# Performance work log

Measured on AMD Instinct MI355X. Metric: run time of the kernel, lower is better.

The kernel has to match this reference:

```python
import jax, jax.numpy as jnp
import numpy as np


def _linear(x, W, b):
    # torch nn.Linear: y = x @ W.T + b, W is [out, in]
    return x @ W.T + b


def _sage_layer(x, edge_index, Ws, bs, Wn, bn):
    # GraphSAGE: mean-aggregate neighbor features via scatter-add, then two linears.
    src, tgt = edge_index[0], edge_index[1]
    N = x.shape[0]
    agg = jax.ops.segment_sum(x[src], tgt, num_segments=N)            # [N, D]
    deg = jax.ops.segment_sum(jnp.ones(src.shape, x.dtype), tgt, num_segments=N)  # [N]
    neighbor_mean = agg / jnp.maximum(deg, 1.0)[:, None]
    return _linear(x, Ws, bs) + _linear(neighbor_mean, Wn, bn)


def setup_inputs() -> dict:
    key = jax.random.key(0)
    ks = jax.random.split(key, 16)
    N, ATTR, H, OUT, E = 50000, 125, 128, 128, 800000
    IN = ATTR + 3
    s = 0.05
    inp = {
        "attr_features": jax.random.normal(ks[0], (N, ATTR), jnp.float32),
        "clustering_coefficient": jax.random.uniform(ks[1], (N, 1), jnp.float32),
        "bidirectional_links_ratio": jax.random.uniform(ks[2], (N, 1), jnp.float32),
        "exist_nodes": jnp.ones((N,), jnp.float32),
        "W_in": s * jax.random.normal(ks[3], (H, IN), jnp.float32),
        "b_in": s * jax.random.normal(ks[4], (H,), jnp.float32),
        "W1_self": s * jax.random.normal(ks[5], (H, H), jnp.float32),
        "b1_self": s * jax.random.normal(ks[6], (H,), jnp.float32),
        "W1_neigh": s * jax.random.normal(ks[7], (H, H), jnp.float32),
        "b1_neigh": s * jax.random.normal(ks[8], (H,), jnp.float32),
        "W2_self": s * jax.random.normal(ks[9], (OUT, H), jnp.float32),
        "b2_self": s * jax.random.normal(ks[10], (OUT,), jnp.float32),
        "W2_neigh": s * jax.random.normal(ks[11], (OUT, H), jnp.float32),
        "b2_neigh": s * jax.random.normal(ks[12], (OUT,), jnp.float32),
        "edge_index": jax.random.randint(ks[13], (2, E), 0, N, jnp.int64),
    }
    return inp


def reference(attr_features, clustering_coefficient, bidirectional_links_ratio,
              exist_nodes, W_in, b_in, W1_self, b1_self, W1_neigh, b1_neigh,
              W2_self, b2_self, W2_neigh, b2_neigh, edge_index):
    exist_col = exist_nodes[:, None]                                   # [N, 1]
    x = jnp.concatenate(
        [attr_features, clustering_coefficient, bidirectional_links_ratio, exist_col],
        axis=1)                                                        # [N, attr_dim+3]
    x = jax.nn.relu(_linear(x, W_in, b_in))                            # dropout=0 -> identity
    x = _sage_layer(x, edge_index, W1_self, b1_self, W1_neigh, b1_neigh)
    x = jax.nn.relu(x)
    x = x * exist_col
    x = _sage_layer(x, edge_index, W2_self, b2_self, W2_neigh, b2_neigh)
    return x * exist_col
```

## Files before the change

kernel.cpp:

```cpp
#include <hip/hip_runtime.h>

typedef __attribute__((ext_vector_type(8))) short short8;
typedef __attribute__((ext_vector_type(4))) float floatx4;

__device__ inline unsigned short f2bf(float f) {
    unsigned u = __float_as_uint(f);
    u += 0x7fffu + ((u >> 16) & 1u);
    return (unsigned short)(u >> 16);
}

__device__ inline short8 pack8(const float4 a, const float4 b) {
    short8 r;
    r[0] = (short)f2bf(a.x); r[1] = (short)f2bf(a.y);
    r[2] = (short)f2bf(a.z); r[3] = (short)f2bf(a.w);
    r[4] = (short)f2bf(b.x); r[5] = (short)f2bf(b.y);
    r[6] = (short)f2bf(b.z); r[7] = (short)f2bf(b.w);
    return r;
}

#define CHUNK_CAP 6144
#define BTILE 4096


__global__ __launch_bounds__(256, 3) void gemm0_bin(
    const float* __restrict__ attr, const float* __restrict__ cc,
    const float* __restrict__ bl, const float* __restrict__ ex,
    const float* __restrict__ Wf, const float* __restrict__ bias,
    unsigned short* __restrict__ out_bf,
    const int* __restrict__ e, int* __restrict__ cursor,
    unsigned* __restrict__ packed_out,
    int N, int ATTR, int E, int nbin) {
    __shared__ __align__(16) char smem[2 * BTILE * 4 + 4 * 256 * 4];
    int t = threadIdx.x;

    if ((int)blockIdx.x < nbin) {
        unsigned* buf  = (unsigned*)smem;
        unsigned* sbuf = buf + BTILE;
        int* hist  = (int*)(sbuf + BTILE);
        int* offs  = hist + 256;
        int* gbase = offs + 256;
        int* lcur  = gbase + 256;
        int e0 = blockIdx.x * BTILE;
        int cnt = min(BTILE, E - e0);
        hist[t] = 0;
        __syncthreads();
        for (int j = t; j < cnt; j += 256) {
            unsigned src = (unsigned)e[e0 + j];
            unsigned tgt = (unsigned)e[E + e0 + j];
            buf[j] = (src << 16) | tgt;
            atomicAdd(&hist[tgt >> 8], 1);
        }
        __syncthreads();
        offs[t] = hist[t];
        __syncthreads();
        for (int o = 1; o < 256; o <<= 1) {
            int v = (t >= o) ? offs[t - o] : 0;
            __syncthreads();
            offs[t] += v;
            __syncthreads();
        }
        int excl = offs[t] - hist[t];
        offs[t] = excl;
        lcur[t] = excl;
        gbase[t] = (hist[t] > 0) ? t * CHUNK_CAP + atomicAdd(&cursor[t], hist[t]) : 0;
        __syncthreads();
        for (int j = t; j < cnt; j += 256) {
            unsigned v = buf[j];
            int c = (v >> 8) & 0xFF;
            int p = atomicAdd(&lcur[c], 1);
            sbuf[p] = v;
        }
        __syncthreads();
        int wv = t >> 6, lane = t & 63;
        for (int c = wv; c < 256; c += 4) {
            int n = hist[c], lo = offs[c], gb = gbase[c];
            for (int j = lane; j < n; j += 64)
                packed_out[gb + j] = sbuf[lo + j];
        }
        return;
    }

    unsigned short* lx = (unsigned short*)smem;
    int lane = t & 63;
    int w = t >> 6;
    int node0 = ((int)blockIdx.x - nbin) * 64;
    int n_off = w * 32;
    int q = lane >> 4;
    int m16 = lane & 15;

    short8 bf[2][4];
    #pragma unroll
    for (int nt = 0; nt < 2; ++nt)
        #pragma unroll
        for (int kk = 0; kk < 4; ++kk) {
            const float* p = Wf + (n_off + nt * 16 + m16) * 128 + kk * 32 + q * 8;
            bf[nt][kk] = pack8(*(const float4*)p, *(const float4*)(p + 4));
        }

    floatx4 acc[4][2];
    #pragma unroll
    for (int nt = 0; nt < 2; ++nt) {
        float bv = bias[n_off + nt * 16 + m16];
        floatx4 b4 = {bv, bv, bv, bv};
        #pragma unroll
        for (int mt = 0; mt < 4; ++mt) acc[mt][nt] = b4;
    }

    for (int i = 0; i < 32; ++i) {
        int idx = t + 256 * i;
        int nd = idx >> 7, col = idx & 127;
        int row = node0 + nd;
        float v = 0.0f;
        if (row < N) {
            if (col < ATTR)           v = attr[(size_t)row * ATTR + col];
            else if (col == ATTR)     v = cc[row];
            else if (col == ATTR + 1) v = bl[row];
            else                      v = ex[row];
        }
        lx[nd * 136 + col] = f2bf(v);
    }
    __syncthreads();

    #pragma unroll
    for (int kk = 0; kk < 4; ++kk) {
        short8 a[4];
        #pragma unroll
        for (int mt = 0; mt < 4; ++mt)
            a[mt] = *(const short8*)(lx + (mt * 16 + m16) * 136 + kk * 32 + q * 8);
        #pragma unroll
        for (int mt = 0; mt < 4; ++mt) {
            acc[mt][0] = __builtin_amdgcn_mfma_f32_16x16x32_bf16(a[mt], bf[0][kk], acc[mt][0], 0, 0, 0);
            acc[mt][1] = __builtin_amdgcn_mfma_f32_16x16x32_bf16(a[mt], bf[1][kk], acc[mt][1], 0, 0, 0);
        }
    }

    for (int mt = 0; mt < 4; ++mt) {
        int rbase = node0 + mt * 16 + q * 4;
        for (int r = 0; r < 4; ++r) {
            int rr = rbase + r;
            if (rr >= N) continue;
            for (int nt = 0; nt < 2; ++nt) {
                float v = fmaxf(acc[mt][nt][r], 0.0f);
                out_bf[(size_t)rr * 128 + n_off + nt * 16 + m16] = f2bf(v);
            }
        }
    }
}


__global__ __launch_bounds__(256) void chunk_csr(const unsigned* __restrict__ packed,
                                                 const int* __restrict__ cursor,
                                                 uint2* __restrict__ rows2,
                                                 int* __restrict__ colv, int N) {
    __shared__ int hist[256], offs[256], lcnt[256];
    __shared__ int sbuf[CHUNK_CAP];
    int c = blockIdx.x;
    int base = c * CHUNK_CAP;
    int cnt = cursor[c];
    int t = threadIdx.x;
    hist[t] = 0;
    __syncthreads();
    for (int j = t; j < cnt; j += 256)
        atomicAdd(&hist[packed[base + j] & 255u], 1);
    __syncthreads();
    offs[t] = hist[t];
    __syncthreads();
    for (int o = 1; o < 256; o <<= 1) {
        int v = (t >= o) ? offs[t - o] : 0;
        __syncthreads();
        offs[t] += v;
        __syncthreads();
    }
    int excl = offs[t] - hist[t];
    offs[t] = excl;
    lcnt[t] = 0;
    __syncthreads();
    int node = c * 256 + t;
    if (node < N) {
        uint2 r;
        r.x = base + excl;
        r.y = base + excl + hist[t];
        rows2[node] = r;
    }
    for (int j = t; j < cnt; j += 256) {
        unsigned v = packed[base + j];
        int nd = v & 255u;
        int p = offs[nd] + atomicAdd(&lcnt[nd], 1);
        sbuf[p] = v >> 16;
    }
    __syncthreads();
    for (int j = t; j < cnt; j += 256) colv[base + j] = sbuf[j];
}


__global__ __launch_bounds__(256) void agg_mean(const unsigned short* __restrict__ x,
                                                const uint2* __restrict__ rows2,
                                                const int* __restrict__ colv,
                                                unsigned short* __restrict__ nm, int N) {
    int wid = (blockIdx.x * 256 + threadIdx.x) >> 6;
    int lane = threadIdx.x & 63;
    if (wid >= N) return;
    uint2 r = rows2[wid];
    int s0 = r.x, s1 = r.y;
    int deg = s1 - s0;
    int mn = deg < 64 ? deg : 64;
    int cvec = (lane < mn) ? colv[s0 + lane] : 0;
    int quarter = lane >> 4;
    int cl = (lane & 15) * 8;
    float a0 = 0.f, a1 = 0.f, a2 = 0.f, a3 = 0.f;
    float a4 = 0.f, a5 = 0.f, a6 = 0.f, a7 = 0.f;
    int lim = mn - 1;
    for (int j = 0; j < mn; j += 32) {
        uint4 v[8];
        #pragma unroll
        for (int u = 0; u < 8; ++u) {
            int ei = j + 4 * u + quarter;
            int idx = (ei <= lim) ? ei : lim;
            int s = __shfl(cvec, idx, 64);
            v[u] = *(const uint4*)(x + (size_t)s * 128 + cl);
        }
        #pragma unroll
        for (int u = 0; u < 8; ++u) {
            int ei = j + 4 * u + quarter;
            if (ei <= lim) {
                a0 += __uint_as_float(v[u].x << 16);
                a1 += __uint_as_float(v[u].x & 0xffff0000u);
                a2 += __uint_as_float(v[u].y << 16);
                a3 += __uint_as_float(v[u].y & 0xffff0000u);
                a4 += __uint_as_float(v[u].z << 16);
                a5 += __uint_as_float(v[u].z & 0xffff0000u);
                a6 += __uint_as_float(v[u].w << 16);
                a7 += __uint_as_float(v[u].w & 0xffff0000u);
            }
        }
    }
    for (int e = s0 + 64; e < s1; e += 4) {
        int ei = e + quarter;
        int idx = (ei < s1) ? ei : s1 - 1;
        int s = colv[idx];
        uint4 v = *(const uint4*)(x + (size_t)s * 128 + cl);
        if (ei < s1) {
            a0 += __uint_as_float(v.x << 16);
            a1 += __uint_as_float(v.x & 0xffff0000u);
            a2 += __uint_as_float(v.y << 16);
            a3 += __uint_as_float(v.y & 0xffff0000u);
            a4 += __uint_as_float(v.z << 16);
            a5 += __uint_as_float(v.z & 0xffff0000u);
            a6 += __uint_as_float(v.w << 16);
            a7 += __uint_as_float(v.w & 0xffff0000u);
        }
    }
    a0 += __shfl_xor(a0, 16, 64); a0 += __shfl_xor(a0, 32, 64);
    a1 += __shfl_xor(a1, 16, 64); a1 += __shfl_xor(a1, 32, 64);
    a2 += __shfl_xor(a2, 16, 64); a2 += __shfl_xor(a2, 32, 64);
    a3 += __shfl_xor(a3, 16, 64); a3 += __shfl_xor(a3, 32, 64);
    a4 += __shfl_xor(a4, 16, 64); a4 += __shfl_xor(a4, 32, 64);
    a5 += __shfl_xor(a5, 16, 64); a5 += __shfl_xor(a5, 32, 64);
    a6 += __shfl_xor(a6, 16, 64); a6 += __shfl_xor(a6, 32, 64);
    a7 += __shfl_xor(a7, 16, 64); a7 += __shfl_xor(a7, 32, 64);
    if (quarter == 0) {
        float inv = 1.0f / (float)(deg > 1 ? deg : 1);
        a0 *= inv; a1 *= inv; a2 *= inv; a3 *= inv;
        a4 *= inv; a5 *= inv; a6 *= inv; a7 *= inv;
        uint4 o;
        o.x = ((unsigned)f2bf(a1) << 16) | (unsigned)f2bf(a0);
        o.y = ((unsigned)f2bf(a3) << 16) | (unsigned)f2bf(a2);
        o.z = ((unsigned)f2bf(a5) << 16) | (unsigned)f2bf(a4);
        o.w = ((unsigned)f2bf(a7) << 16) | (unsigned)f2bf(a6);
        *(uint4*)(nm + (size_t)wid * 128 + cl) = o;
    }
}


__global__ __launch_bounds__(256, 3) void gemm_fused(
    const unsigned short* __restrict__ X0, const unsigned short* __restrict__ X1,
    const float* __restrict__ W0f, const float* __restrict__ W1f,
    const float* __restrict__ b0, const float* __restrict__ b1,
    const float* __restrict__ ex,
    unsigned short* __restrict__ obf, float* __restrict__ of32,
    int N, int relu) {
    __shared__ unsigned short lx[64 * 136];
    int tid = threadIdx.x;
    int lane = tid & 63;
    int w = tid >> 6;
    int node0 = blockIdx.x * 64;
    int n_off = w * 32;
    int q = lane >> 4;
    int m16 = lane & 15;

    short8 bf0[2][4], bf1[2][4];
    #pragma unroll
    for (int nt = 0; nt < 2; ++nt)
        #pragma unroll
        for (int kk = 0; kk < 4; ++kk) {
            const float* p0 = W0f + (n_off + nt * 16 + m16) * 128 + kk * 32 + q * 8;
            bf0[nt][kk] = pack8(*(const float4*)p0, *(const float4*)(p0 + 4));
            const float* p1 = W1f + (n_off + nt * 16 + m16) * 128 + kk * 32 + q * 8;
            bf1[nt][kk] = pack8(*(const float4*)p1, *(const float4*)(p1 + 4));
        }

    floatx4 acc[4][2];
    #pragma unroll
    for (int nt = 0; nt < 2; ++nt) {
        int col = n_off + nt * 16 + m16;
        float bv = b0[col] + b1[col];
        floatx4 b4 = {bv, bv, bv, bv};
        #pragma unroll
        for (int mt = 0; mt < 4; ++mt) acc[mt][nt] = b4;
    }

    for (int ph = 0; ph < 2; ++ph) {
        const unsigned short* X = ph ? X1 : X0;
        for (int i = 0; i < 4; ++i) {
            int c = tid + 256 * i;
            int nd = c >> 4, ck = c & 15;
            short8 v = {0, 0, 0, 0, 0, 0, 0, 0};
            if (node0 + nd < N) v = *(const short8*)(X + (size_t)(node0 + nd) * 128 + ck * 8);
            *(short8*)(lx + nd * 136 + ck * 8) = v;
        }
        __syncthreads();
        #pragma unroll
        for (int kk = 0; kk < 4; ++kk) {
            short8 a[4];
            #pragma unroll
            for (int mt = 0; mt < 4; ++mt)
                a[mt] = *(const short8*)(lx + (mt * 16 + m16) * 136 + kk * 32 + q * 8);
            #pragma unroll
            for (int mt = 0; mt < 4; ++mt) {
                const short8* p0 = ph ? &bf1[0][kk] : &bf0[0][kk];
                const short8* p1 = ph ? &bf1[1][kk] : &bf0[1][kk];
                acc[mt][0] = __builtin_amdgcn_mfma_f32_16x16x32_bf16(a[mt], *p0, acc[mt][0], 0, 0, 0);
                acc[mt][1] = __builtin_amdgcn_mfma_f32_16x16x32_bf16(a[mt], *p1, acc[mt][1], 0, 0, 0);
            }
        }
        __syncthreads();
    }

    for (int mt = 0; mt < 4; ++mt) {
        int rbase = node0 + mt * 16 + q * 4;
        for (int r = 0; r < 4; ++r) {
            int rr = rbase + r;
            if (rr >= N) continue;
            float e = ex ? ex[rr] : 1.0f;
            for (int nt = 0; nt < 2; ++nt) {
                float v = acc[mt][nt][r];
                if (relu) v = fmaxf(v, 0.0f);
                v *= e;
                int col = n_off + nt * 16 + m16;
                if (obf) obf[(size_t)rr * 128 + col] = f2bf(v);
                else     of32[(size_t)rr * 128 + col] = v;
            }
        }
    }
}


extern "C" void kernel_launch(void* const* d_in, const int* in_sizes, int n_in,
                              void* d_out, int out_size, void* d_ws, size_t ws_size,
                              hipStream_t stream) {
    const float* attr = (const float*)d_in[0];
    const float* cc   = (const float*)d_in[1];
    const float* bl   = (const float*)d_in[2];
    const float* ex   = (const float*)d_in[3];
    const float* w_in = (const float*)d_in[4];
    const float* b_in = (const float*)d_in[5];
    const float* w1s  = (const float*)d_in[6];
    const float* b1s  = (const float*)d_in[7];
    const float* w1n  = (const float*)d_in[8];
    const float* b1n  = (const float*)d_in[9];
    const float* w2s  = (const float*)d_in[10];
    const float* b2s  = (const float*)d_in[11];
    const float* w2n  = (const float*)d_in[12];
    const float* b2n  = (const float*)d_in[13];
    const int*   eidx = (const int*)d_in[14];

    int N = in_sizes[3];
    int ATTR = in_sizes[0] / N;
    int E = in_sizes[14] / 2;
    int Npad = ((N + 63) / 64) * 64;
    int nchunk = (N + 255) / 256;
    int ntilesE = (E + BTILE - 1) / BTILE;
    int gblk = Npad / 64;

    char* ws = (char*)d_ws;
    size_t off = 0;
    auto alloc = [&](size_t bytes) -> char* {
        off = (off + 255) & ~(size_t)255;
        char* p = ws + off;
        off += bytes;
        return p;
    };
    unsigned short* x1 = (unsigned short*)alloc((size_t)Npad * 128 * 2);
    unsigned short* x2 = (unsigned short*)alloc((size_t)Npad * 128 * 2);
    unsigned short* nm = (unsigned short*)alloc((size_t)Npad * 128 * 2);
    int* colv        = (int*)alloc((size_t)nchunk * CHUNK_CAP * 4);
    unsigned* packed = (unsigned*)alloc((size_t)nchunk * CHUNK_CAP * 4);
    uint2* rows2     = (uint2*)alloc((size_t)N * 8);
    int* cursor      = (int*)alloc(256 * 4);

    hipMemsetAsync(cursor, 0, 256 * sizeof(int), stream);

    gemm0_bin<<<ntilesE + gblk, 256, 0, stream>>>(attr, cc, bl, ex, w_in, b_in, x1,
                                                  eidx, cursor, packed,
                                                  N, ATTR, E, ntilesE);
    chunk_csr<<<nchunk, 256, 0, stream>>>(packed, cursor, rows2, colv, N);
    agg_mean<<<(N + 3) / 4, 256, 0, stream>>>(x1, rows2, colv, nm, N);
    gemm_fused<<<gblk, 256, 0, stream>>>(x1, nm, w1s, w1n, b1s, b1n, ex,
                                         x2, (float*)nullptr, N, 1);
    agg_mean<<<(N + 3) / 4, 256, 0, stream>>>(x2, rows2, colv, nm, N);
    gemm_fused<<<gblk, 256, 0, stream>>>(x2, nm, w2s, w2n, b2s, b2n, ex,
                                         (unsigned short*)nullptr, (float*)d_out, N, 0);
}
```

Before: 264.4 us.

## Widen CSR chunks, persist binning blocks, pre-convert weights, stage attr rows

Edge binning now uses 128 chunks of 512 nodes with a new packed encoding, and a fixed pool of at most 256 blocks loops over the edge tiles. The chunk_csr kernel builds 512-node CSR rows with a two-per-thread scan. Extra blocks in the first kernel convert the layer weights to bf16 once and pre-sum the biases, so the fused GEMMs load short8 directly instead of converting per block. The input GEMM stages attr rows into LDS with coalesced float4 loads instead of strided scalar reads. This raises LDS use per block, which may lower occupancy.

```diff
diff --git a/kernel.cpp b/kernel.cpp
--- a/kernel.cpp
+++ b/kernel.cpp
@@ -9,17 +9,9 @@
     return (unsigned short)(u >> 16);
 }
 
-__device__ inline short8 pack8(const float4 a, const float4 b) {
-    short8 r;
-    r[0] = (short)f2bf(a.x); r[1] = (short)f2bf(a.y);
-    r[2] = (short)f2bf(a.z); r[3] = (short)f2bf(a.w);
-    r[4] = (short)f2bf(b.x); r[5] = (short)f2bf(b.y);
-    r[6] = (short)f2bf(b.z); r[7] = (short)f2bf(b.w);
-    return r;
-}
-
-#define CHUNK_CAP 6144
+#define CHUNK_CAP 12288
 #define BTILE 4096
+#define NPREP 256
 
 
 __global__ __launch_bounds__(256, 3) void gemm0_bin(
@@ -29,72 +21,114 @@
     unsigned short* __restrict__ out_bf,
     const int* __restrict__ e, int* __restrict__ cursor,
     unsigned* __restrict__ packed_out,
-    int N, int ATTR, int E, int nbin) {
-    __shared__ __align__(16) char smem[2 * BTILE * 4 + 4 * 256 * 4];
+    const float* __restrict__ w1s, const float* __restrict__ w1n,
+    const float* __restrict__ w2s, const float* __restrict__ w2n,
+    const float* __restrict__ b1s, const float* __restrict__ b1n,
+    const float* __restrict__ b2s, const float* __restrict__ b2n,
+    unsigned short* __restrict__ wb, float* __restrict__ biasf,
+    int N, int ATTR, int E, int ntilesE, int nbin) {
+    __shared__ __align__(16) char smem[49408];
     int t = threadIdx.x;
-
-    if ((int)blockIdx.x < nbin) {
+    int bid = blockIdx.x;
+
+    if (bid < nbin) {
         unsigned* buf  = (unsigned*)smem;
         unsigned* sbuf = buf + BTILE;
         int* hist  = (int*)(sbuf + BTILE);
-        int* offs  = hist + 256;
-        int* gbase = offs + 256;
-        int* lcur  = gbase + 256;
-        int e0 = blockIdx.x * BTILE;
-        int cnt = min(BTILE, E - e0);
-        hist[t] = 0;
-        __syncthreads();
-        for (int j = t; j < cnt; j += 256) {
-            unsigned src = (unsigned)e[e0 + j];
-            unsigned tgt = (unsigned)e[E + e0 + j];
-            buf[j] = (src << 16) | tgt;
-            atomicAdd(&hist[tgt >> 8], 1);
-        }
-        __syncthreads();
-        offs[t] = hist[t];
-        __syncthreads();
-        for (int o = 1; o < 256; o <<= 1) {
-            int v = (t >= o) ? offs[t - o] : 0;
-            __syncthreads();
-            offs[t] += v;
-            __syncthreads();
-        }
-        int excl = offs[t] - hist[t];
-        offs[t] = excl;
-        lcur[t] = excl;
-        gbase[t] = (hist[t] > 0) ? t * CHUNK_CAP + atomicAdd(&cursor[t], hist[t]) : 0;
-        __syncthreads();
-        for (int j = t; j < cnt; j += 256) {
-            unsigned v = buf[j];
-            int c = (v >> 8) & 0xFF;
-            int p = atomicAdd(&lcur[c], 1);
-            sbuf[p] = v;
-        }
-        __syncthreads();
-        int wv = t >> 6, lane = t & 63;
-        for (int c = wv; c < 256; c += 4) {
-            int n = hist[c], lo = offs[c], gb = gbase[c];
-            for (int j = lane; j < n; j += 64)
-                packed_out[gb + j] = sbuf[lo + j];
+        int* offs  = hist + 128;
+        int* gbase = offs + 128;
+        int* lcur  = gbase + 128;
+        for (int tile = bid; tile < ntilesE; tile += nbin) {
+            int e0 = tile * BTILE;
+            int cnt = min(BTILE, E - e0);
+            if (t < 128) hist[t] = 0;
+            __syncthreads();
+            for (int j = t; j < cnt; j += 256) {
+                unsigned src = (unsigned)e[e0 + j];
+                unsigned tgt = (unsigned)e[E + e0 + j];
+                unsigned c = tgt >> 9;
+                buf[j] = (c << 25) | (src << 9) | (tgt & 511u);
+                atomicAdd(&hist[c], 1);
+            }
+            __syncthreads();
+            if (t < 128) offs[t] = hist[t];
+            __syncthreads();
+            for (int o = 1; o < 128; o <<= 1) {
+                int v = (t < 128 && t >= o) ? offs[t - o] : 0;
+                __syncthreads();
+                if (t < 128) offs[t] += v;
+                __syncthreads();
+            }
+            if (t < 128) {
+                int excl = offs[t] - hist[t];
+                offs[t] = excl;
+                lcur[t] = excl;
+                gbase[t] = (hist[t] > 0) ? t * CHUNK_CAP + atomicAdd(&cursor[t], hist[t]) : 0;
+            }
+            __syncthreads();
+            for (int j = t; j < cnt; j += 256) {
+                unsigned v = buf[j];
+                int c = v >> 25;
+                int p = atomicAdd(&lcur[c], 1);
+                sbuf[p] = v;
+            }
+            __syncthreads();
+            int wv = t >> 6, lane = t & 63;
+            for (int c = wv; c < 128; c += 4) {
+                int n = hist[c], lo = offs[c], gb = gbase[c];
+                for (int j = lane; j < n; j += 64)
+                    packed_out[gb + j] = sbuf[lo + j];
+            }
+            __syncthreads();
         }
         return;
     }
 
-    unsigned short* lx = (unsigned short*)smem;
+    if (bid < nbin + NPREP) {
+        int pb = bid - nbin;
+        int idx = pb * 256 + t;
+        int m = idx >> 14, j = idx & 16383;
+        const float* src = (m == 0) ? w1s : (m == 1) ? w1n : (m == 2) ? w2s : w2n;
+        wb[idx] = f2bf(src[j]);
+        if (pb == 0 && t < 128) {
+            biasf[t]       = b1s[t] + b1n[t];
+            biasf[128 + t] = b2s[t] + b2n[t];
+        }
+        return;
+    }
+
+    float* sflat = (float*)smem;
+    unsigned short* lx = (unsigned short*)(smem + 32000);
     int lane = t & 63;
     int w = t >> 6;
-    int node0 = ((int)blockIdx.x - nbin) * 64;
+    int node0 = (bid - nbin - NPREP) * 64;
     int n_off = w * 32;
     int q = lane >> 4;
     int m16 = lane & 15;
 
+    int nrow = N - node0; nrow = nrow > 64 ? 64 : (nrow < 0 ? 0 : nrow);
+    int nelem = nrow * ATTR;
+    {
+        const float* abase = attr + (size_t)node0 * ATTR;
+        int nv = nelem >> 2;
+        const float4* src4 = (const float4*)abase;
+        for (int i = t; i < nv; i += 256) ((float4*)sflat)[i] = src4[i];
+        for (int i = (nv << 2) + t; i < nelem; i += 256) sflat[i] = abase[i];
+    }
+
     short8 bf[2][4];
     #pragma unroll
     for (int nt = 0; nt < 2; ++nt)
         #pragma unroll
         for (int kk = 0; kk < 4; ++kk) {
             const float* p = Wf + (n_off + nt * 16 + m16) * 128 + kk * 32 + q * 8;
-            bf[nt][kk] = pack8(*(const float4*)p, *(const float4*)(p + 4));
+            float4 aa = *(const float4*)p, bb = *(const float4*)(p + 4);
+            short8 r;
+            r[0] = (short)f2bf(aa.x); r[1] = (short)f2bf(aa.y);
+            r[2] = (short)f2bf(aa.z); r[3] = (short)f2bf(aa.w);
+            r[4] = (short)f2bf(bb.x); r[5] = (short)f2bf(bb.y);
+            r[6] = (short)f2bf(bb.z); r[7] = (short)f2bf(bb.w);
+            bf[nt][kk] = r;
         }
 
     floatx4 acc[4][2];
@@ -105,6 +139,7 @@
         #pragma unroll
         for (int mt = 0; mt < 4; ++mt) acc[mt][nt] = b4;
     }
+    __syncthreads();
 
     for (int i = 0; i < 32; ++i) {
         int idx = t + 256 * i;
@@ -112,7 +147,7 @@
         int row = node0 + nd;
         float v = 0.0f;
         if (row < N) {
-            if (col < ATTR)           v = attr[(size_t)row * ATTR + col];
+            if (col < ATTR)           v = sflat[nd * ATTR + col];
             else if (col == ATTR)     v = cc[row];
             else if (col == ATTR + 1) v = bl[row];
             else                      v = ex[row];
@@ -152,41 +187,47 @@
                                                  const int* __restrict__ cursor,
                                                  uint2* __restrict__ rows2,
                                                  int* __restrict__ colv, int N) {
-    __shared__ int hist[256], offs[256], lcnt[256];
+    __shared__ int hist[512], offs[512], lcnt[512], pp[256];
     __shared__ int sbuf[CHUNK_CAP];
     int c = blockIdx.x;
     int base = c * CHUNK_CAP;
     int cnt = cursor[c];
     int t = threadIdx.x;
     hist[t] = 0;
+    hist[t + 256] = 0;
     __syncthreads();
     for (int j = t; j < cnt; j += 256)
-        atomicAdd(&hist[packed[base + j] & 255u], 1);
-    __syncthreads();
-    offs[t] = hist[t];
+        atomicAdd(&hist[packed[base + j] & 511u], 1);
+    __syncthreads();
+    int a0 = hist[2 * t], a1 = hist[2 * t + 1];
+    pp[t] = a0 + a1;
     __syncthreads();
     for (int o = 1; o < 256; o <<= 1) {
-        int v = (t >= o) ? offs[t - o] : 0;
+        int v = (t >= o) ? pp[t - o] : 0;
         __syncthreads();
-        offs[t] += v;
+        pp[t] += v;
         __syncthreads();
     }
-    int excl = offs[t] - hist[t];
-    offs[t] = excl;
-    lcnt[t] = 0;
-    __syncthreads();
-    int node = c * 256 + t;
-    if (node < N) {
-        uint2 r;
-        r.x = base + excl;
-        r.y = base + excl + hist[t];
-        rows2[node] = r;
+    int excl = pp[t] - (a0 + a1);
+    offs[2 * t] = excl;
+    offs[2 * t + 1] = excl + a0;
+    lcnt[2 * t] = 0;
+    lcnt[2 * t + 1] = 0;
+    __syncthreads();
+    for (int j = t; j < 512; j += 256) {
+        int node = c * 512 + j;
+        if (node < N) {
+            uint2 r;
+            r.x = base + offs[j];
+            r.y = base + offs[j] + hist[j];
+            rows2[node] = r;
+        }
     }
     for (int j = t; j < cnt; j += 256) {
         unsigned v = packed[base + j];
-        int nd = v & 255u;
-        int p = offs[nd] + atomicAdd(&lcnt[nd], 1);
-        sbuf[p] = v >> 16;
+        int node = v & 511u;
+        int p = offs[node] + atomicAdd(&lcnt[node], 1);
+        sbuf[p] = (v >> 9) & 0xFFFFu;
     }
     __syncthreads();
     for (int j = t; j < cnt; j += 256) colv[base + j] = sbuf[j];
@@ -274,9 +315,8 @@
 
 __global__ __launch_bounds__(256, 3) void gemm_fused(
     const unsigned short* __restrict__ X0, const unsigned short* __restrict__ X1,
-    const float* __restrict__ W0f, const float* __restrict__ W1f,
-    const float* __restrict__ b0, const float* __restrict__ b1,
-    const float* __restrict__ ex,
+    const unsigned short* __restrict__ W0, const unsigned short* __restrict__ W1,
+    const float* __restrict__ bias, const float* __restrict__ ex,
     unsigned short* __restrict__ obf, float* __restrict__ of32,
     int N, int relu) {
     __shared__ unsigned short lx[64 * 136];
@@ -293,17 +333,14 @@
     for (int nt = 0; nt < 2; ++nt)
         #pragma unroll
         for (int kk = 0; kk < 4; ++kk) {
-            const float* p0 = W0f + (n_off + nt * 16 + m16) * 128 + kk * 32 + q * 8;
-            bf0[nt][kk] = pack8(*(const float4*)p0, *(const float4*)(p0 + 4));
-            const float* p1 = W1f + (n_off + nt * 16 + m16) * 128 + kk * 32 + q * 8;
-            bf1[nt][kk] = pack8(*(const float4*)p1, *(const float4*)(p1 + 4));
+            bf0[nt][kk] = *(const short8*)(W0 + (n_off + nt * 16 + m16) * 128 + kk * 32 + q * 8);
+            bf1[nt][kk] = *(const short8*)(W1 + (n_off + nt * 16 + m16) * 128 + kk * 32 + q * 8);
         }
 
     floatx4 acc[4][2];
     #pragma unroll
     for (int nt = 0; nt < 2; ++nt) {
-        int col = n_off + nt * 16 + m16;
-        float bv = b0[col] + b1[col];
+        float bv = bias[n_off + nt * 16 + m16];
         floatx4 b4 = {bv, bv, bv, bv};
         #pragma unroll
         for (int mt = 0; mt < 4; ++mt) acc[mt][nt] = b4;
@@ -378,8 +415,9 @@
     int ATTR = in_sizes[0] / N;
     int E = in_sizes[14] / 2;
     int Npad = ((N + 63) / 64) * 64;
-    int nchunk = (N + 255) / 256;
+    int nchunk = (N + 511) / 512;
     int ntilesE = (E + BTILE - 1) / BTILE;
+    int nbin = ntilesE < 256 ? ntilesE : 256;
     int gblk = Npad / 64;
 
     char* ws = (char*)d_ws;
@@ -396,18 +434,23 @@
     int* colv        = (int*)alloc((size_t)nchunk * CHUNK_CAP * 4);
     unsigned* packed = (unsigned*)alloc((size_t)nchunk * CHUNK_CAP * 4);
     uint2* rows2     = (uint2*)alloc((size_t)N * 8);
-    int* cursor      = (int*)alloc(256 * 4);
-
-    hipMemsetAsync(cursor, 0, 256 * sizeof(int), stream);
-
-    gemm0_bin<<<ntilesE + gblk, 256, 0, stream>>>(attr, cc, bl, ex, w_in, b_in, x1,
-                                                  eidx, cursor, packed,
-                                                  N, ATTR, E, ntilesE);
+    int* cursor      = (int*)alloc(128 * 4);
+    unsigned short* wb = (unsigned short*)alloc((size_t)4 * 16384 * 2);
+    float* biasf     = (float*)alloc(256 * 4);
+
+    hipMemsetAsync(cursor, 0, 128 * sizeof(int), stream);
+
+    gemm0_bin<<<nbin + NPREP + gblk, 256, 0, stream>>>(
+        attr, cc, bl, ex, w_in, b_in, x1,
+        eidx, cursor, packed,
+        w1s, w1n, w2s, w2n, b1s, b1n, b2s, b2n, wb, biasf,
+        N, ATTR, E, ntilesE, nbin);
     chunk_csr<<<nchunk, 256, 0, stream>>>(packed, cursor, rows2, colv, N);
     agg_mean<<<(N + 3) / 4, 256, 0, stream>>>(x1, rows2, colv, nm, N);
-    gemm_fused<<<gblk, 256, 0, stream>>>(x1, nm, w1s, w1n, b1s, b1n, ex,
-                                         x2, (float*)nullptr, N, 1);
+    gemm_fused<<<gblk, 256, 0, stream>>>(x1, nm, wb, wb + 16384,
+                                         biasf, ex, x2, (float*)nullptr, N, 1);
     agg_mean<<<(N + 3) / 4, 256, 0, stream>>>(x2, rows2, colv, nm, N);
-    gemm_fused<<<gblk, 256, 0, stream>>>(x2, nm, w2s, w2n, b2s, b2n, ex,
-                                         (unsigned short*)nullptr, (float*)d_out, N, 0);
-}
+    gemm_fused<<<gblk, 256, 0, stream>>>(x2, nm, wb + 2 * 16384, wb + 3 * 16384,
+                                         biasf + 128, ex, (unsigned short*)nullptr,
+                                         (float*)d_out, N, 0);
+}
```

New measurement: 242.1 us. 8.4% less time.
